# Kernel optimization log

Hardware: AMD Instinct MI355X
Metric: run time of the kernel (lower is better)

## Reference

```python
import jax, jax.numpy as jnp
import numpy as np

B, S, E, H = 4, 2048, 1024, 16
D = E // H  # head_dim = 64


def setup_inputs() -> dict:
    key = jax.random.key(0)
    ks = jax.random.split(key, 10)
    scale = 1.0 / np.sqrt(E)
    return {
        "decoder_sequence": jax.random.normal(ks[0], (B, S, E), dtype=jnp.float32),
        # stacked per-head projection weights (math-equivalent to per-head nn.Linear)
        "Wq": jax.random.normal(ks[1], (H, E, D), dtype=jnp.float32) * scale,
        "bq": jnp.zeros((H, D), dtype=jnp.float32),
        "Wk": jax.random.normal(ks[2], (H, E, D), dtype=jnp.float32) * scale,
        "bk": jnp.zeros((H, D), dtype=jnp.float32),
        "Wv": jax.random.normal(ks[3], (H, E, D), dtype=jnp.float32) * scale,
        "bv": jnp.zeros((H, D), dtype=jnp.float32),
        "Wo": jax.random.normal(ks[4], (E, E), dtype=jnp.float32) * scale,
        "bo": jnp.zeros((E,), dtype=jnp.float32),
    }


def reference(decoder_sequence, Wq, bq, Wk, bk, Wv, bv, Wo, bo):
    x = decoder_sequence  # [B,S,E]
    # per-head Q/K/V projections, batched over the head axis
    Q = jnp.einsum('bse,hed->bhsd', x, Wq) + bq[:, None, :]
    K = jnp.einsum('bse,hed->bhsd', x, Wk) + bk[:, None, :]
    V = jnp.einsum('bse,hed->bhsd', x, Wv) + bv[:, None, :]
    # scaled scores with causal mask (upper triangle -> -inf)
    A = jnp.einsum('bhid,bhjd->bhij', Q, K) / jnp.sqrt(jnp.float32(D))
    causal = jnp.tril(jnp.ones((S, S), dtype=bool))  # True where allowed
    A = jnp.where(causal, A, -jnp.inf)
    A = jax.nn.softmax(A, axis=-1)
    Hout = jnp.einsum('bhij,bhjd->bhid', A, V)  # [B,H,S,D]
    # concat heads: [B,S,H*D]
    concat = jnp.transpose(Hout, (0, 2, 1, 3)).reshape(B, S, H * D)
    return concat @ Wo.T + bo
```

## Files before the change

### kernel.cpp

```cpp
#include <hip/hip_runtime.h>
#include <stdint.h>
#include <stddef.h>

typedef __bf16 bf16;
typedef __bf16 bf16x8 __attribute__((ext_vector_type(8)));
typedef __bf16 bf16x4 __attribute__((ext_vector_type(4)));
typedef float  f32x4  __attribute__((ext_vector_type(4)));
typedef float  f32x16 __attribute__((ext_vector_type(16)));
typedef unsigned short ush;
typedef ush ush8 __attribute__((ext_vector_type(8)));
typedef unsigned int uint;

#define B_  4
#define S_  2048
#define E_  1024
#define H_  16
#define D_  64
#define M_  (B_*S_)
#define K_  E_
#define QSCALE 0.18033688011112042f

__device__ __forceinline__ void gload_lds16(const void* g, void* l) {
  __builtin_amdgcn_global_load_lds((const __attribute__((address_space(1))) void*)g,
                                   (__attribute__((address_space(3))) void*)l, 16, 0, 0);
}
__device__ __forceinline__ f32x4 mfma16(bf16x8 a, bf16x8 b, f32x4 c) {
  return __builtin_amdgcn_mfma_f32_16x16x32_bf16(a, b, c, 0, 0, 0);
}
__device__ __forceinline__ f32x16 mfma32(bf16x8 a, bf16x8 b, f32x16 c) {
  return __builtin_amdgcn_mfma_f32_32x32x16_bf16(a, b, c, 0, 0, 0);
}
__device__ __forceinline__ int swz4(int row, int ch) { return ch ^ ((row >> 1) & 3); }
__device__ __forceinline__ uint cvtpk(float lo, float hi) {
  uint r;
  asm("v_cvt_pk_bf16_f32 %0, %1, %2" : "=v"(r) : "v"(lo), "v"(hi));
  return r;
}

__global__ void cast_f32_bf16(const float* __restrict__ src, bf16* __restrict__ dst, int n4) {
  int idx = blockIdx.x * blockDim.x + threadIdx.x;
  int stride = gridDim.x * blockDim.x;
  for (int i = idx; i < n4; i += stride) {
    float4 v = ((const float4*)src)[i];
    union { bf16 b[4]; ushort4 u; } cv;
    cv.b[0] = (bf16)v.x; cv.b[1] = (bf16)v.y; cv.b[2] = (bf16)v.z; cv.b[3] = (bf16)v.w;
    ((ushort4*)dst)[i] = cv.u;
  }
}

__global__ void pack_w_t(const float* __restrict__ Wq, const float* __restrict__ Wk,
                         const float* __restrict__ Wv, bf16* __restrict__ Wp) {
  __shared__ float t[64][65];
  const int tid = threadIdx.x;
  const int wh = blockIdx.y;
  const int which = wh >> 4, h = wh & 15;
  const int e0 = blockIdx.x << 6;
  const float* src = (which == 0) ? Wq : (which == 1 ? Wk : Wv);
  src += (size_t)h * (E_ * D_);
  #pragma unroll
  for (int i = 0; i < 4; ++i) {
    int fi = tid + 256 * i;
    int e = fi >> 4, c = fi & 15;
    float4 v = *(const float4*)(src + (size_t)(e0 + e) * D_ + c * 4);
    t[c * 4 + 0][e] = v.x; t[c * 4 + 1][e] = v.y;
    t[c * 4 + 2][e] = v.z; t[c * 4 + 3][e] = v.w;
  }
  __syncthreads();
  #pragma unroll
  for (int i = 0; i < 2; ++i) {
    int cid = tid + 256 * i;
    int d = cid >> 3, cc = cid & 7;
    ush8 o;
    #pragma unroll
    for (int j = 0; j < 8; ++j) {
      union { bf16 b; ush u; } cv; cv.b = (bf16)t[d][cc * 8 + j]; o[j] = cv.u;
    }
    *(ush8*)(Wp + ((size_t)which * 1024 + h * 64 + d) * K_ + e0 + cc * 8) = o;
  }
}

template <int MODE>
__launch_bounds__(256, 2)
__global__ void gemm_kernel(const bf16* __restrict__ A, const bf16* __restrict__ Bm,
                            int Ntot,
                            const float* __restrict__ bias0, const float* __restrict__ bias1,
                            const float* __restrict__ bias2,
                            bf16* __restrict__ Qo, bf16* __restrict__ Ko, bf16* __restrict__ Vo,
                            float* __restrict__ Fo) {
  __shared__ __align__(16) bf16 lds_a[2][128 * 32];
  __shared__ __align__(16) bf16 lds_b[2][128 * 32];
  const int tid = threadIdx.x;
  const int lane = tid & 63;
  const int w = tid >> 6;
  const int wr = w >> 1, wc = w & 1;
  const int nblk = Ntot >> 7;
  const int mt = blockIdx.x / nblk, nt = blockIdx.x % nblk;
  const int m0 = mt << 7, n0 = nt << 7;

  f32x4 acc[4][4] = {};

  auto stage = [&](int buf, int kt) {
    #pragma unroll
    for (int i = 0; i < 2; ++i) {
      int cb = (w * 2 + i) * 64;
      int cid = cb + lane;
      int row = cid >> 2, cir = cid & 3;
      int lch = swz4(row, cir);
      const bf16* ga = A  + (size_t)(m0 + row) * K_ + kt * 32 + lch * 8;
      const bf16* gb = Bm + (size_t)(n0 + row) * K_ + kt * 32 + lch * 8;
      gload_lds16(ga, &lds_a[buf][cb * 8]);
      gload_lds16(gb, &lds_b[buf][cb * 8]);
    }
  };

  const int NT = K_ / 32;
  stage(0, 0);
  for (int kt = 0; kt < NT; ++kt) {
    if (kt + 1 < NT) stage((kt + 1) & 1, kt + 1);
    __syncthreads();
    const bf16x8* pa = (const bf16x8*)&lds_a[kt & 1][0];
    const bf16x8* pb = (const bf16x8*)&lds_b[kt & 1][0];
    bf16x8 af[4], bfr[4];
    #pragma unroll
    for (int mb = 0; mb < 4; ++mb) {
      int row = wr * 64 + mb * 16 + (lane & 15);
      af[mb] = pa[row * 4 + swz4(row, lane >> 4)];
    }
    #pragma unroll
    for (int nb = 0; nb < 4; ++nb) {
      int row = wc * 64 + nb * 16 + (lane & 15);
      bfr[nb] = pb[row * 4 + swz4(row, lane >> 4)];
    }
    #pragma unroll
    for (int mb = 0; mb < 4; ++mb)
      #pragma unroll
      for (int nb = 0; nb < 4; ++nb)
        acc[mb][nb] = mfma16(af[mb], bfr[nb], acc[mb][nb]);
    __syncthreads();
  }

  #pragma unroll
  for (int mb = 0; mb < 4; ++mb) {
    #pragma unroll
    for (int nb = 0; nb < 4; ++nb) {
      #pragma unroll
      for (int r = 0; r < 4; ++r) {
        int mi = m0 + wr * 64 + mb * 16 + (lane >> 4) * 4 + r;
        int ni = n0 + wc * 64 + nb * 16 + (lane & 15);
        float v = acc[mb][nb][r];
        if (MODE == 0) {
          int which = ni >> 10;
          int col = ni & 1023;
          const float* bp = (which == 0) ? bias0 : (which == 1 ? bias1 : bias2);
          v += bp[col];
          if (which == 0) v *= QSCALE;
          int h = col >> 6, d = col & 63;
          int b = mi >> 11, s = mi & 2047;
          bf16* dst = (which == 0) ? Qo : (which == 1 ? Ko : Vo);
          dst[(((size_t)(b * H_ + h)) * S_ + s) * D_ + d] = (bf16)v;
        } else {
          Fo[(size_t)mi * E_ + ni] = v + bias0[ni];
        }
      }
    }
  }
}

__global__ void transpose_v(const bf16* __restrict__ V, bf16* __restrict__ Vt) {
  __shared__ ush t[64 * 65];
  const int bh = blockIdx.y;
  const int s0 = blockIdx.x * 64;
  const int tid = threadIdx.x;
  #pragma unroll
  for (int i = 0; i < 2; ++i) {
    int cid = tid + 256 * i;
    int r = cid >> 3, c = cid & 7;
    ush8 val = *(const ush8*)(V + ((size_t)bh * S_ + s0 + r) * D_ + c * 8);
    #pragma unroll
    for (int j = 0; j < 8; ++j) t[(c * 8 + j) * 65 + r] = val[j];
  }
  __syncthreads();
  #pragma unroll
  for (int i = 0; i < 2; ++i) {
    int cid = tid + 256 * i;
    int d = cid >> 3, sc = cid & 7;
    ush8 o;
    #pragma unroll
    for (int j = 0; j < 8; ++j) o[j] = t[d * 65 + sc * 8 + j];
    *(ush8*)(Vt + ((size_t)bh * D_ + d) * S_ + s0 + sc * 8) = o;
  }
}

struct QTile {
  bf16x8 qf[4];
  f32x16 oacc[2];
  float m, l;
};

__device__ __forceinline__ void init_q(QTile& S, const bf16* qrow, int hi) {
  #pragma unroll
  for (int kc = 0; kc < 4; ++kc)
    S.qf[kc] = *(const bf16x8*)(qrow + (2 * kc + hi) * 8);
  #pragma unroll
  for (int r = 0; r < 16; ++r) { S.oacc[0][r] = 0.f; S.oacc[1][r] = 0.f; }
  S.m = -1e30f; S.l = 0.f;
}

__device__ __forceinline__ void tile_step(QTile& S, const bf16* klds, const bf16* vlds,
                                          int kv0, int qb_, int qg_, int hi, int ln) {
  if (kv0 > qb_ + 31) return;
  f32x16 s0 = {}, s1 = {};
  #pragma unroll
  for (int kc = 0; kc < 4; ++kc) {
    int ch = (2 * kc + hi) ^ (ln & 7);
    bf16x8 k0 = *(const bf16x8*)&klds[ln * 64 + ch * 8];
    bf16x8 k1 = *(const bf16x8*)&klds[(32 + ln) * 64 + ch * 8];
    s0 = mfma32(k0, S.qf[kc], s0);
    s1 = mfma32(k1, S.qf[kc], s1);
  }
  if (kv0 + 63 > qb_) {
    #pragma unroll
    for (int r = 0; r < 16; ++r) {
      int crow = (r & 3) + 8 * (r >> 2) + 4 * hi;
      if (kv0 + crow > qg_)      s0[r] = -1e30f;
      if (kv0 + 32 + crow > qg_) s1[r] = -1e30f;
    }
  }
  float mt_ = s0[0];
  #pragma unroll
  for (int r = 1; r < 16; ++r) mt_ = fmaxf(mt_, s0[r]);
  #pragma unroll
  for (int r = 0; r < 16; ++r) mt_ = fmaxf(mt_, s1[r]);
  mt_ = fmaxf(mt_, __shfl_xor(mt_, 32, 64));
  bool resc = mt_ > S.m + 8.f;
  float mnew = resc ? mt_ : S.m;
  float alpha = resc ? exp2f(S.m - mnew) : 1.f;
  S.m = mnew;
  float rs = 0.f;
  #pragma unroll
  for (int r = 0; r < 16; ++r) { float p = exp2f(s0[r] - mnew); s0[r] = p; rs += p; }
  #pragma unroll
  for (int r = 0; r < 16; ++r) { float p = exp2f(s1[r] - mnew); s1[r] = p; rs += p; }
  rs += __shfl_xor(rs, 32, 64);
  S.l = S.l * alpha + rs;
  if (__any(resc)) {
    #pragma unroll
    for (int r = 0; r < 16; ++r) { S.oacc[0][r] *= alpha; S.oacc[1][r] *= alpha; }
  }
  bf16x8 pf[4];
  #pragma unroll
  for (int mtl = 0; mtl < 2; ++mtl) {
    #pragma unroll
    for (int c = 0; c < 2; ++c) {
      const f32x16& p = mtl ? s1 : s0;
      uint wa = cvtpk(p[8 * c + 0], p[8 * c + 1]);
      uint wb = cvtpk(p[8 * c + 2], p[8 * c + 3]);
      uint wcx = cvtpk(p[8 * c + 4], p[8 * c + 5]);
      uint wd = cvtpk(p[8 * c + 6], p[8 * c + 7]);
      asm("v_permlane32_swap_b32 %0, %1" : "+v"(wa), "+v"(wcx));
      asm("v_permlane32_swap_b32 %0, %1" : "+v"(wb), "+v"(wd));
      union { uint u[4]; bf16x8 v; } cvt;
      cvt.u[0] = wa; cvt.u[1] = wb; cvt.u[2] = wcx; cvt.u[3] = wd;
      pf[mtl * 2 + c] = cvt.v;
    }
  }
  #pragma unroll
  for (int dm = 0; dm < 2; ++dm) {
    #pragma unroll
    for (int ks = 0; ks < 4; ++ks) {
      int row = dm * 32 + ln;
      int ch = (2 * ks + hi) ^ (ln & 7);
      bf16x8 vf = *(const bf16x8*)&vlds[row * 64 + ch * 8];
      oaccum:
      S.oacc[dm] = mfma32(vf, pf[ks], S.oacc[dm]);
    }
  }
}

__device__ __forceinline__ void store_o(const QTile& S, bf16* orow, int hi) {
  float rinv = 1.f / S.l;
  #pragma unroll
  for (int dm = 0; dm < 2; ++dm) {
    #pragma unroll
    for (int g = 0; g < 4; ++g) {
      bf16x4 st;
      #pragma unroll
      for (int i = 0; i < 4; ++i) st[i] = (bf16)(S.oacc[dm][4 * g + i] * rinv);
      *(bf16x4*)(orow + dm * 32 + g * 8 + hi * 4) = st;
    }
  }
}

__launch_bounds__(256, 2)
__global__ void attn_kernel(const bf16* __restrict__ Q, const bf16* __restrict__ K,
                            const bf16* __restrict__ Vt, bf16* __restrict__ Oc) {
  __shared__ __align__(16) bf16 k_lds[2][64 * 64];
  __shared__ __align__(16) bf16 v_lds[2][64 * 64];
  const int tid = threadIdx.x, lane = tid & 63, w = tid >> 6;
  const int hi = lane >> 5, ln = lane & 31;
  const int bid = blockIdx.x;
  const int bh = (bid & 7) | ((bid >> 6) << 3);
  const int x  = (bid >> 3) & 7;
  const int jta = x, jtb = 15 - x;
  const int qba = (jta << 7) + w * 32, qbb = (jtb << 7) + w * 32;
  const int qga = qba + ln, qgb = qbb + ln;
  const int nta = 2 * jta + 2, ntb = 2 * jtb + 2;

  QTile A, B;
  init_q(A, Q + ((size_t)bh * S_ + qga) * D_, hi);
  init_q(B, Q + ((size_t)bh * S_ + qgb) * D_, hi);

  auto stage = [&](int buf, int t) {
    const int kv0 = t << 6;
    #pragma unroll
    for (int i = 0; i < 2; ++i) {
      int cb = (w * 2 + i) * 64;
      int cid = cb + lane;
      int row = cid >> 3, cir = cid & 7;
      int lch = cir ^ (row & 7);
      gload_lds16(K  + ((size_t)bh * S_ + kv0 + row) * D_ + lch * 8, &k_lds[buf][cb * 8]);
      gload_lds16(Vt + ((size_t)bh * D_ + row) * S_ + kv0 + lch * 8, &v_lds[buf][cb * 8]);
    }
  };

  stage(0, 0);
  __syncthreads();
  for (int t = 0; t < ntb; ++t) {
    const int cur = t & 1;
    if (t + 1 < ntb) stage(cur ^ 1, t + 1);
    const int kv0 = t << 6;
    if (t < nta) tile_step(A, k_lds[cur], v_lds[cur], kv0, qba, qga, hi, ln);
    tile_step(B, k_lds[cur], v_lds[cur], kv0, qbb, qgb, hi, ln);
    __syncthreads();
  }

  const int b = bh >> 4, h = bh & 15;
  store_o(A, Oc + ((size_t)(b * S_ + qga)) * E_ + h * D_, hi);
  store_o(B, Oc + ((size_t)(b * S_ + qgb)) * E_ + h * D_, hi);
}

extern "C" void kernel_launch(void* const* d_in, const int* in_sizes, int n_in,
                              void* d_out, int out_size, void* d_ws, size_t ws_size,
                              hipStream_t stream) {
  const float* x  = (const float*)d_in[0];
  const float* Wq = (const float*)d_in[1];
  const float* bq = (const float*)d_in[2];
  const float* Wk = (const float*)d_in[3];
  const float* bk = (const float*)d_in[4];
  const float* Wv = (const float*)d_in[5];
  const float* bv = (const float*)d_in[6];
  const float* Wo = (const float*)d_in[7];
  const float* bo = (const float*)d_in[8];
  float* out = (float*)d_out;

  uint8_t* ws = (uint8_t*)d_ws;
  bf16* Xbf   = (bf16*)(ws + 0);
  bf16* Wpack = (bf16*)(ws + 16777216);
  bf16* Wot   = (bf16*)(ws + 23068672);
  bf16* Qb    = (bf16*)(ws + 25165824);
  bf16* Kb    = (bf16*)(ws + 41943040);
  bf16* Vb    = (bf16*)(ws + 58720256);
  bf16* Vtb   = (bf16*)(ws + 75497472);
  bf16* Cc    = Xbf;

  cast_f32_bf16<<<2048, 256, 0, stream>>>(x,  Xbf, (M_ * K_) / 4);
  cast_f32_bf16<<<1024, 256, 0, stream>>>(Wo, Wot, (E_ * E_) / 4);
  pack_w_t<<<dim3(16, 48), 256, 0, stream>>>(Wq, Wk, Wv, Wpack);

  gemm_kernel<0><<<dim3(64 * 24), 256, 0, stream>>>(Xbf, Wpack, 3072, bq, bk, bv,
                                                    Qb, Kb, Vb, nullptr);
  transpose_v<<<dim3(S_ / 64, B_ * H_), 256, 0, stream>>>(Vb, Vtb);

  attn_kernel<<<512, 256, 0, stream>>>(Qb, Kb, Vtb, Cc);

  gemm_kernel<1><<<dim3(64 * 8), 256, 0, stream>>>(Cc, Wot, 1024, bo, nullptr, nullptr,
                                                   nullptr, nullptr, nullptr, out);
}
```

Baseline: 198.5 us.

## Replace LDS-staged attention with single-wave blocks loading K/V from global

The attention kernel no longer stages K and V tiles into shared memory with double buffering and block-wide barriers. Each 64-thread block now handles one pair of 32-row query tiles (p and 63-p, balancing causal work) and reads K and V fragments directly from global memory into registers. This removes LDS traffic and synchronisation and raises the block count, but the K/V tiles that four waves used to share are now fetched separately by each wave, relying on L2 for reuse. Register pressure from holding the K/V fragments may also rise.

```diff
diff --git a/kernel.cpp b/kernel.cpp
--- a/kernel.cpp
+++ b/kernel.cpp
@@ -206,19 +206,32 @@
   S.m = -1e30f; S.l = 0.f;
 }
 
-__device__ __forceinline__ void tile_step(QTile& S, const bf16* klds, const bf16* vlds,
-                                          int kv0, int qb_, int qg_, int hi, int ln) {
-  if (kv0 > qb_ + 31) return;
+__device__ __forceinline__ void tile_step_g(QTile& S, const bf16* __restrict__ Kb,
+                                            const bf16* __restrict__ Vb,
+                                            int kv0, int qu, int qg_, int hi, int ln) {
+  const bf16* kr0 = Kb + (size_t)(kv0 + ln) * D_;
+  const bf16* kr1 = Kb + (size_t)(kv0 + 32 + ln) * D_;
+  bf16x8 k0[4], k1[4];
+  #pragma unroll
+  for (int kc = 0; kc < 4; ++kc) {
+    k0[kc] = *(const bf16x8*)(kr0 + (2 * kc + hi) * 8);
+    k1[kc] = *(const bf16x8*)(kr1 + (2 * kc + hi) * 8);
+  }
+  bf16x8 vf[2][4];
+  #pragma unroll
+  for (int dm = 0; dm < 2; ++dm) {
+    const bf16* vr = Vb + (size_t)(dm * 32 + ln) * S_ + kv0;
+    #pragma unroll
+    for (int ks = 0; ks < 4; ++ks)
+      vf[dm][ks] = *(const bf16x8*)(vr + (2 * ks + hi) * 8);
+  }
   f32x16 s0 = {}, s1 = {};
   #pragma unroll
   for (int kc = 0; kc < 4; ++kc) {
-    int ch = (2 * kc + hi) ^ (ln & 7);
-    bf16x8 k0 = *(const bf16x8*)&klds[ln * 64 + ch * 8];
-    bf16x8 k1 = *(const bf16x8*)&klds[(32 + ln) * 64 + ch * 8];
-    s0 = mfma32(k0, S.qf[kc], s0);
-    s1 = mfma32(k1, S.qf[kc], s1);
-  }
-  if (kv0 + 63 > qb_) {
+    s0 = mfma32(k0[kc], S.qf[kc], s0);
+    s1 = mfma32(k1[kc], S.qf[kc], s1);
+  }
+  if (kv0 + 63 > qu) {
     #pragma unroll
     for (int r = 0; r < 16; ++r) {
       int crow = (r & 3) + 8 * (r >> 2) + 4 * hi;
@@ -265,16 +278,10 @@
     }
   }
   #pragma unroll
-  for (int dm = 0; dm < 2; ++dm) {
-    #pragma unroll
-    for (int ks = 0; ks < 4; ++ks) {
-      int row = dm * 32 + ln;
-      int ch = (2 * ks + hi) ^ (ln & 7);
-      bf16x8 vf = *(const bf16x8*)&vlds[row * 64 + ch * 8];
-      oaccum:
-      S.oacc[dm] = mfma32(vf, pf[ks], S.oacc[dm]);
-    }
-  }
+  for (int dm = 0; dm < 2; ++dm)
+    #pragma unroll
+    for (int ks = 0; ks < 4; ++ks)
+      S.oacc[dm] = mfma32(vf[dm][ks], pf[ks], S.oacc[dm]);
 }
 
 __device__ __forceinline__ void store_o(const QTile& S, bf16* orow, int hi) {
@@ -291,52 +298,27 @@
   }
 }
 
-__launch_bounds__(256, 2)
+__launch_bounds__(64, 3)
 __global__ void attn_kernel(const bf16* __restrict__ Q, const bf16* __restrict__ K,
                             const bf16* __restrict__ Vt, bf16* __restrict__ Oc) {
-  __shared__ __align__(16) bf16 k_lds[2][64 * 64];
-  __shared__ __align__(16) bf16 v_lds[2][64 * 64];
-  const int tid = threadIdx.x, lane = tid & 63, w = tid >> 6;
-  const int hi = lane >> 5, ln = lane & 31;
-  const int bid = blockIdx.x;
-  const int bh = (bid & 7) | ((bid >> 6) << 3);
-  const int x  = (bid >> 3) & 7;
-  const int jta = x, jtb = 15 - x;
-  const int qba = (jta << 7) + w * 32, qbb = (jtb << 7) + w * 32;
-  const int qga = qba + ln, qgb = qbb + ln;
-  const int nta = 2 * jta + 2, ntb = 2 * jtb + 2;
-
-  QTile A, B;
-  init_q(A, Q + ((size_t)bh * S_ + qga) * D_, hi);
-  init_q(B, Q + ((size_t)bh * S_ + qgb) * D_, hi);
-
-  auto stage = [&](int buf, int t) {
-    const int kv0 = t << 6;
-    #pragma unroll
-    for (int i = 0; i < 2; ++i) {
-      int cb = (w * 2 + i) * 64;
-      int cid = cb + lane;
-      int row = cid >> 3, cir = cid & 7;
-      int lch = cir ^ (row & 7);
-      gload_lds16(K  + ((size_t)bh * S_ + kv0 + row) * D_ + lch * 8, &k_lds[buf][cb * 8]);
-      gload_lds16(Vt + ((size_t)bh * D_ + row) * S_ + kv0 + lch * 8, &v_lds[buf][cb * 8]);
-    }
-  };
-
-  stage(0, 0);
-  __syncthreads();
-  for (int t = 0; t < ntb; ++t) {
-    const int cur = t & 1;
-    if (t + 1 < ntb) stage(cur ^ 1, t + 1);
-    const int kv0 = t << 6;
-    if (t < nta) tile_step(A, k_lds[cur], v_lds[cur], kv0, qba, qga, hi, ln);
-    tile_step(B, k_lds[cur], v_lds[cur], kv0, qbb, qgb, hi, ln);
-    __syncthreads();
-  }
-
+  const int tid = threadIdx.x, hi = tid >> 5, ln = tid & 31;
+  const int i = blockIdx.x;
+  const int bh = (i & 7) | ((i >> 8) << 3);
+  const int p = (i >> 3) & 31;
+  const bf16* Kb = K  + (size_t)bh * S_ * D_;
+  const bf16* Vb = Vt + (size_t)bh * D_ * S_;
   const int b = bh >> 4, h = bh & 15;
-  store_o(A, Oc + ((size_t)(b * S_ + qga)) * E_ + h * D_, hi);
-  store_o(B, Oc + ((size_t)(b * S_ + qgb)) * E_ + h * D_, hi);
+
+  for (int half = 0; half < 2; ++half) {
+    const int u = half ? (63 - p) : p;
+    const int qu = u * 32;
+    QTile S;
+    init_q(S, Q + ((size_t)bh * S_ + qu + ln) * D_, hi);
+    const int ntl = (u >> 1) + 1;
+    for (int t = 0; t < ntl; ++t)
+      tile_step_g(S, Kb, Vb, t * 64, qu, qu + ln, hi, ln);
+    store_o(S, Oc + ((size_t)(b * S_ + qu + ln)) * E_ + h * D_, hi);
+  }
 }
 
 extern "C" void kernel_launch(void* const* d_in, const int* in_sizes, int n_in,
@@ -371,7 +353,7 @@
                                                     Qb, Kb, Vb, nullptr);
   transpose_v<<<dim3(S_ / 64, B_ * H_), 256, 0, stream>>>(Vb, Vtb);
 
-  attn_kernel<<<512, 256, 0, stream>>>(Qb, Kb, Vtb, Cc);
+  attn_kernel<<<2048, 64, 0, stream>>>(Qb, Kb, Vtb, Cc);
 
   gemm_kernel<1><<<dim3(64 * 8), 256, 0, stream>>>(Cc, Wot, 1024, bo, nullptr, nullptr,
                                                    nullptr, nullptr, nullptr, out);
```

After: 262.1 us. 1.32x slower.

## Split attention KV range across two blocks, fuse V transpose into QKV GEMM

Applied to the files above, without the earlier changes.

The attention kernel now splits each query tile's KV range into two halves handled by separate blocks (1024 blocks instead of 512). Each block writes unnormalized partial outputs plus m/l statistics, and a new merge kernel combines them. The aim is more parallelism and better load balance on the GPU. The QKV GEMM epilogue also writes V directly in transposed layout, which removes the separate transpose kernel, and the GEMM grid is remapped with a block swizzle for cache locality. In exchange, the partial buffers add extra memory traffic, the merge adds a kernel launch, and the transposed V stores are only 4-wide and strided.

```diff
diff --git a/kernel.cpp b/kernel.cpp
--- a/kernel.cpp
+++ b/kernel.cpp
@@ -85,7 +85,7 @@
                             int Ntot,
                             const float* __restrict__ bias0, const float* __restrict__ bias1,
                             const float* __restrict__ bias2,
-                            bf16* __restrict__ Qo, bf16* __restrict__ Ko, bf16* __restrict__ Vo,
+                            bf16* __restrict__ Qo, bf16* __restrict__ Ko, bf16* __restrict__ Vto,
                             float* __restrict__ Fo) {
   __shared__ __align__(16) bf16 lds_a[2][128 * 32];
   __shared__ __align__(16) bf16 lds_b[2][128 * 32];
@@ -94,7 +94,9 @@
   const int w = tid >> 6;
   const int wr = w >> 1, wc = w & 1;
   const int nblk = Ntot >> 7;
-  const int mt = blockIdx.x / nblk, nt = blockIdx.x % nblk;
+  const int qch = gridDim.x >> 3;
+  const int swz = (blockIdx.x & 7) * qch + (blockIdx.x >> 3);
+  const int mt = swz / nblk, nt = swz % nblk;
   const int m0 = mt << 7, n0 = nt << 7;
 
   f32x4 acc[4][4] = {};
@@ -143,51 +145,34 @@
   for (int mb = 0; mb < 4; ++mb) {
     #pragma unroll
     for (int nb = 0; nb < 4; ++nb) {
-      #pragma unroll
-      for (int r = 0; r < 4; ++r) {
-        int mi = m0 + wr * 64 + mb * 16 + (lane >> 4) * 4 + r;
-        int ni = n0 + wc * 64 + nb * 16 + (lane & 15);
-        float v = acc[mb][nb][r];
-        if (MODE == 0) {
-          int which = ni >> 10;
-          int col = ni & 1023;
-          const float* bp = (which == 0) ? bias0 : (which == 1 ? bias1 : bias2);
-          v += bp[col];
-          if (which == 0) v *= QSCALE;
-          int h = col >> 6, d = col & 63;
-          int b = mi >> 11, s = mi & 2047;
-          bf16* dst = (which == 0) ? Qo : (which == 1 ? Ko : Vo);
-          dst[(((size_t)(b * H_ + h)) * S_ + s) * D_ + d] = (bf16)v;
+      const int ni  = n0 + wc * 64 + nb * 16 + (lane & 15);
+      const int mi0 = m0 + wr * 64 + mb * 16 + (lane >> 4) * 4;
+      if (MODE == 0) {
+        const int which = ni >> 10;
+        const int col = ni & 1023;
+        const float* bp = (which == 0) ? bias0 : (which == 1 ? bias1 : bias2);
+        const float bv = bp[col];
+        const int hh = col >> 6, d = col & 63;
+        const int b = mi0 >> 11, s0r = mi0 & 2047;
+        if (which == 2) {
+          bf16x4 st;
+          #pragma unroll
+          for (int r = 0; r < 4; ++r) st[r] = (bf16)(acc[mb][nb][r] + bv);
+          *(bf16x4*)(Vto + ((size_t)((b * H_ + hh) * D_ + d)) * S_ + s0r) = st;
         } else {
-          Fo[(size_t)mi * E_ + ni] = v + bias0[ni];
+          bf16* dst = (which == 0) ? Qo : Ko;
+          const float sc = (which == 0) ? QSCALE : 1.f;
+          #pragma unroll
+          for (int r = 0; r < 4; ++r)
+            dst[(((size_t)(b * H_ + hh)) * S_ + (s0r + r)) * D_ + d] =
+                (bf16)((acc[mb][nb][r] + bv) * sc);
         }
+      } else {
+        #pragma unroll
+        for (int r = 0; r < 4; ++r)
+          Fo[(size_t)(mi0 + r) * E_ + ni] = acc[mb][nb][r] + bias0[ni];
       }
     }
-  }
-}
-
-__global__ void transpose_v(const bf16* __restrict__ V, bf16* __restrict__ Vt) {
-  __shared__ ush t[64 * 65];
-  const int bh = blockIdx.y;
-  const int s0 = blockIdx.x * 64;
-  const int tid = threadIdx.x;
-  #pragma unroll
-  for (int i = 0; i < 2; ++i) {
-    int cid = tid + 256 * i;
-    int r = cid >> 3, c = cid & 7;
-    ush8 val = *(const ush8*)(V + ((size_t)bh * S_ + s0 + r) * D_ + c * 8);
-    #pragma unroll
-    for (int j = 0; j < 8; ++j) t[(c * 8 + j) * 65 + r] = val[j];
-  }
-  __syncthreads();
-  #pragma unroll
-  for (int i = 0; i < 2; ++i) {
-    int cid = tid + 256 * i;
-    int d = cid >> 3, sc = cid & 7;
-    ush8 o;
-    #pragma unroll
-    for (int j = 0; j < 8; ++j) o[j] = t[d * 65 + sc * 8 + j];
-    *(ush8*)(Vt + ((size_t)bh * D_ + d) * S_ + s0 + sc * 8) = o;
   }
 }
 
@@ -271,7 +256,6 @@
       int row = dm * 32 + ln;
       int ch = (2 * ks + hi) ^ (ln & 7);
       bf16x8 vf = *(const bf16x8*)&vlds[row * 64 + ch * 8];
-      oaccum:
       S.oacc[dm] = mfma32(vf, pf[ks], S.oacc[dm]);
     }
   }
@@ -291,24 +275,39 @@
   }
 }
 
+__device__ __forceinline__ void store_part(const QTile& S, bf16* prow, float* pml, int hi) {
+  #pragma unroll
+  for (int dm = 0; dm < 2; ++dm) {
+    #pragma unroll
+    for (int g = 0; g < 4; ++g) {
+      bf16x4 st;
+      #pragma unroll
+      for (int i = 0; i < 4; ++i) st[i] = (bf16)S.oacc[dm][4 * g + i];
+      *(bf16x4*)(prow + dm * 32 + g * 8 + hi * 4) = st;
+    }
+  }
+  if (hi == 0) { pml[0] = S.m; pml[1] = S.l; }
+}
+
 __launch_bounds__(256, 2)
 __global__ void attn_kernel(const bf16* __restrict__ Q, const bf16* __restrict__ K,
-                            const bf16* __restrict__ Vt, bf16* __restrict__ Oc) {
+                            const bf16* __restrict__ Vt, bf16* __restrict__ Cc,
+                            bf16* __restrict__ Po, float* __restrict__ Pml, int nh) {
   __shared__ __align__(16) bf16 k_lds[2][64 * 64];
   __shared__ __align__(16) bf16 v_lds[2][64 * 64];
   const int tid = threadIdx.x, lane = tid & 63, w = tid >> 6;
   const int hi = lane >> 5, ln = lane & 31;
   const int bid = blockIdx.x;
-  const int bh = (bid & 7) | ((bid >> 6) << 3);
-  const int x  = (bid >> 3) & 7;
+  const int bh = bid & 63;
+  const int rest = bid >> 6;
+  const int x = rest & 7;
+  const int h = (nh == 2) ? (rest >> 3) : 0;
   const int jta = x, jtb = 15 - x;
-  const int qba = (jta << 7) + w * 32, qbb = (jtb << 7) + w * 32;
-  const int qga = qba + ln, qgb = qbb + ln;
-  const int nta = 2 * jta + 2, ntb = 2 * jtb + 2;
-
-  QTile A, B;
-  init_q(A, Q + ((size_t)bh * S_ + qga) * D_, hi);
-  init_q(B, Q + ((size_t)bh * S_ + qgb) * D_, hi);
+  const int lenA = (2 * x + 2) / nh, lenB = (32 - 2 * x) / nh;
+  const int ta0 = h * lenA, ta1 = ta0 + lenA;
+  const int tb0 = h * lenB, tb1 = tb0 + lenB;
+  const bf16* Kb = K  + (size_t)bh * (S_ * D_);
+  const bf16* Vb = Vt + (size_t)bh * (D_ * S_);
 
   auto stage = [&](int buf, int t) {
     const int kv0 = t << 6;
@@ -318,25 +317,71 @@
       int cid = cb + lane;
       int row = cid >> 3, cir = cid & 7;
       int lch = cir ^ (row & 7);
-      gload_lds16(K  + ((size_t)bh * S_ + kv0 + row) * D_ + lch * 8, &k_lds[buf][cb * 8]);
-      gload_lds16(Vt + ((size_t)bh * D_ + row) * S_ + kv0 + lch * 8, &v_lds[buf][cb * 8]);
+      gload_lds16(Kb + (size_t)(kv0 + row) * D_ + lch * 8, &k_lds[buf][cb * 8]);
+      gload_lds16(Vb + (size_t)row * S_ + kv0 + lch * 8, &v_lds[buf][cb * 8]);
     }
   };
 
-  stage(0, 0);
-  __syncthreads();
-  for (int t = 0; t < ntb; ++t) {
-    const int cur = t & 1;
-    if (t + 1 < ntb) stage(cur ^ 1, t + 1);
-    const int kv0 = t << 6;
-    if (t < nta) tile_step(A, k_lds[cur], v_lds[cur], kv0, qba, qga, hi, ln);
-    tile_step(B, k_lds[cur], v_lds[cur], kv0, qbb, qgb, hi, ln);
+  QTile SA, SB;
+  const int sA = jta * 128 + w * 32 + ln, sB = jtb * 128 + w * 32 + ln;
+  init_q(SA, Q + ((size_t)bh * S_ + sA) * D_, hi);
+  init_q(SB, Q + ((size_t)bh * S_ + sB) * D_, hi);
+
+  {
+    const int qb_ = jta * 128 + w * 32, qg_ = qb_ + ln;
+    stage(0, ta0);
     __syncthreads();
-  }
-
-  const int b = bh >> 4, h = bh & 15;
-  store_o(A, Oc + ((size_t)(b * S_ + qga)) * E_ + h * D_, hi);
-  store_o(B, Oc + ((size_t)(b * S_ + qgb)) * E_ + h * D_, hi);
+    for (int t = ta0; t < ta1; ++t) {
+      int cur = (t - ta0) & 1;
+      if (t + 1 < ta1) stage(cur ^ 1, t + 1);
+      tile_step(SA, k_lds[cur], v_lds[cur], t * 64, qb_, qg_, hi, ln);
+      __syncthreads();
+    }
+  }
+  {
+    const int qb_ = jtb * 128 + w * 32, qg_ = qb_ + ln;
+    stage(0, tb0);
+    __syncthreads();
+    for (int t = tb0; t < tb1; ++t) {
+      int cur = (t - tb0) & 1;
+      if (t + 1 < tb1) stage(cur ^ 1, t + 1);
+      tile_step(SB, k_lds[cur], v_lds[cur], t * 64, qb_, qg_, hi, ln);
+      __syncthreads();
+    }
+  }
+
+  if (nh == 2) {
+    size_t ra = (size_t)(h * 64 + bh) * 2048 + sA;
+    size_t rb = (size_t)(h * 64 + bh) * 2048 + sB;
+    store_part(SA, Po + ra * 64, Pml + ra * 2, hi);
+    store_part(SB, Po + rb * 64, Pml + rb * 2, hi);
+  } else {
+    const int b = bh >> 4, hh = bh & 15;
+    store_o(SA, Cc + ((size_t)(b * S_ + sA)) * E_ + hh * D_, hi);
+    store_o(SB, Cc + ((size_t)(b * S_ + sB)) * E_ + hh * D_, hi);
+  }
+}
+
+__global__ void attn_merge(const bf16* __restrict__ Po, const float* __restrict__ Pml,
+                           bf16* __restrict__ Cc) {
+  const int idx = blockIdx.x * 256 + threadIdx.x;
+  const int rg = idx >> 3, oct = idx & 7;
+  const int bh = rg >> 11, s = rg & 2047;
+  const size_t r0 = (size_t)bh * 2048 + s;
+  const size_t r1 = (size_t)(64 + bh) * 2048 + s;
+  const float m0 = Pml[r0 * 2], l0 = Pml[r0 * 2 + 1];
+  const float m1 = Pml[r1 * 2], l1 = Pml[r1 * 2 + 1];
+  const float mx = fmaxf(m0, m1);
+  const float a0 = exp2f(m0 - mx), a1 = exp2f(m1 - mx);
+  const float rl = 1.f / (l0 * a0 + l1 * a1);
+  const bf16x8 v0 = *(const bf16x8*)(Po + r0 * 64 + oct * 8);
+  const bf16x8 v1 = *(const bf16x8*)(Po + r1 * 64 + oct * 8);
+  bf16x8 o;
+  #pragma unroll
+  for (int j = 0; j < 8; ++j)
+    o[j] = (bf16)(((float)v0[j] * a0 + (float)v1[j] * a1) * rl);
+  const int b = bh >> 4, hh = bh & 15;
+  *(bf16x8*)(Cc + ((size_t)(b * S_ + s)) * E_ + hh * D_ + oct * 8) = o;
 }
 
 extern "C" void kernel_launch(void* const* d_in, const int* in_sizes, int n_in,
@@ -359,19 +404,22 @@
   bf16* Wot   = (bf16*)(ws + 23068672);
   bf16* Qb    = (bf16*)(ws + 25165824);
   bf16* Kb    = (bf16*)(ws + 41943040);
-  bf16* Vb    = (bf16*)(ws + 58720256);
   bf16* Vtb   = (bf16*)(ws + 75497472);
   bf16* Cc    = Xbf;
+  bf16*  Po  = (bf16*)(ws + 92274688);
+  float* Pml = (float*)(ws + 125829120);
+  const bool split = (ws_size >= 127926272ull);
+  const int nh = split ? 2 : 1;
 
   cast_f32_bf16<<<2048, 256, 0, stream>>>(x,  Xbf, (M_ * K_) / 4);
   cast_f32_bf16<<<1024, 256, 0, stream>>>(Wo, Wot, (E_ * E_) / 4);
   pack_w_t<<<dim3(16, 48), 256, 0, stream>>>(Wq, Wk, Wv, Wpack);
 
   gemm_kernel<0><<<dim3(64 * 24), 256, 0, stream>>>(Xbf, Wpack, 3072, bq, bk, bv,
-                                                    Qb, Kb, Vb, nullptr);
-  transpose_v<<<dim3(S_ / 64, B_ * H_), 256, 0, stream>>>(Vb, Vtb);
-
-  attn_kernel<<<512, 256, 0, stream>>>(Qb, Kb, Vtb, Cc);
+                                                    Qb, Kb, Vtb, nullptr);
+
+  attn_kernel<<<dim3(512 * nh), 256, 0, stream>>>(Qb, Kb, Vtb, Cc, Po, Pml, nh);
+  if (split) attn_merge<<<dim3(4096), 256, 0, stream>>>(Po, Pml, Cc);
 
   gemm_kernel<1><<<dim3(64 * 8), 256, 0, stream>>>(Cc, Wot, 1024, bo, nullptr, nullptr,
                                                    nullptr, nullptr, nullptr, out);
```

After: 199.9 us. No clear change (+0.7%).
